# Kernel tuning notes

Hardware: AMD Instinct MI355X
Metric: run time of the kernel (lower is better)

## Reference

```python
import jax, jax.numpy as jnp
import numpy as np

N = 100000   # nodes
E = 1600000  # edges
H = 2        # heads
F = 64       # out_feats per head
D = 256      # node feature dim
DE = 8       # edge feature dim
NEG_SLOPE = 0.2


def setup_inputs() -> dict:
    key = jax.random.key(0)
    ks = jax.random.split(key, 12)
    s = 0.05
    return {
        "feat_src": jax.random.normal(ks[0], (N, D), jnp.float32),
        "feat_edge": jax.random.normal(ks[1], (E, DE), jnp.float32),
        "edge_src": jax.random.randint(ks[2], (E,), 0, N, jnp.int32),
        "edge_dst": jax.random.randint(ks[3], (E,), 0, N, jnp.int32),
        "W_src": jax.random.normal(ks[4], (H * F, D), jnp.float32) * s,
        "W_dst": jax.random.normal(ks[5], (H * F, D), jnp.float32) * s,
        "b_dst": jax.random.normal(ks[6], (H * F,), jnp.float32) * s,
        "W_attn_src": jax.random.normal(ks[7], (H, D), jnp.float32) * s,
        "W_attn_dst": jax.random.normal(ks[8], (H, D), jnp.float32) * s,
        "W_attn_edge": jax.random.normal(ks[9], (H, DE), jnp.float32) * s,
        "W_ngnn": jax.random.normal(ks[10], (H * F, H * F), jnp.float32) * s,
        "b_ngnn": jax.random.normal(ks[11], (H * F,), jnp.float32) * s,
    }


def reference(feat_src, feat_edge, edge_src, edge_dst,
              W_src, W_dst, b_dst, W_attn_src, W_attn_dst, W_attn_edge,
              W_ngnn, b_ngnn):
    # node projections (graph is not a block -> feat_dst = feat_src)
    h_src = (feat_src @ W_src.T).reshape(N, H, F)          # [N,H,F]
    h_dst = (feat_src @ W_dst.T + b_dst).reshape(N, H, F)  # residual branch

    # per-node attention logits [N,H]
    a_src = feat_src @ W_attn_src.T
    a_dst = feat_src @ W_attn_dst.T
    a_edge = feat_edge @ W_attn_edge.T                     # [E,H]

    # per-edge score: u_add_v + edge term, LeakyReLU
    e = a_src[edge_src] + a_dst[edge_dst] + a_edge         # [E,H]
    e = jnp.where(e >= 0, e, NEG_SLOPE * e)

    # edge softmax over incoming edges of each destination node
    m = jax.ops.segment_max(e, edge_dst, num_segments=N)   # [N,H]
    ex = jnp.exp(e - m[edge_dst])
    z = jax.ops.segment_sum(ex, edge_dst, num_segments=N)  # [N,H]
    a = ex / z[edge_dst]                                   # [E,H]

    # weighted gather-scatter aggregation: u_mul_e -> sum per dst
    msg = h_src[edge_src] * a[:, :, None]                  # [E,H,F]
    rst = jax.ops.segment_sum(msg, edge_dst, num_segments=N)  # [N,H,F]

    # ngnn layer + ReLU
    rst = rst.reshape(N, H * F)
    rst = jax.nn.relu(rst @ W_ngnn.T + b_ngnn)
    rst = rst.reshape(N, H, F)

    # residual connection via dst_fc
    rst = rst + h_dst
    return rst
```

## Files before the change

### kernel.cpp

```cpp
#include <hip/hip_runtime.h>
#include <hip/hip_bf16.h>
#include <math.h>

#define NN 100000
#define EE 1600000
#define DD 256
#define DEE 8
#define HF 128
#define NEG_SLOPE 0.2f
#define NBUCK 196
#define P1_EPB 1024

typedef __bf16 bf16x8 __attribute__((ext_vector_type(8)));
typedef float  f32x4  __attribute__((ext_vector_type(4)));

__device__ inline ushort f2bf(float f) {
    uint32_t x = __builtin_bit_cast(uint32_t, f);
    x += 0x7fffu + ((x >> 16) & 1u);
    return (ushort)(x >> 16);
}
__device__ inline float bf2f(ushort u) {
    uint32_t x = ((uint32_t)u) << 16;
    return __builtin_bit_cast(float, x);
}
__device__ inline float u2f(uint u) { return __builtin_bit_cast(float, u); }
__device__ inline uint f2u(float f) { return __builtin_bit_cast(uint, f); }
__device__ inline float lo_bf(uint p) { return __builtin_bit_cast(float, p << 16); }
__device__ inline float hi_bf(uint p) { return __builtin_bit_cast(float, p & 0xffff0000u); }

__device__ inline void load_lds16(const void* g, void* l) {
    __builtin_amdgcn_global_load_lds(
        (const __attribute__((address_space(1))) void*)g,
        (__attribute__((address_space(3))) void*)l, 16, 0, 0);
}

__global__ __launch_bounds__(256) void f2bf3_kernel(
    const float* __restrict__ wa, const float* __restrict__ wb,
    const float* __restrict__ wc,
    ushort* __restrict__ oa, ushort* __restrict__ ob, ushort* __restrict__ oc)
{
    int i = (blockIdx.x * 256 + threadIdx.x) * 4;
    const int na = HF * DD, nb2 = 2 * HF * DD, nc3 = 2 * HF * DD + HF * HF;
    const float* src; ushort* dst; int o;
    if (i < na)       { src = wa; dst = oa; o = i; }
    else if (i < nb2) { src = wb; dst = ob; o = i - na; }
    else if (i < nc3) { src = wc; dst = oc; o = i - nb2; }
    else return;
    float4 v = *(const float4*)(src + o);
    ushort4 u;
    u.x = f2bf(v.x); u.y = f2bf(v.y); u.z = f2bf(v.z); u.w = f2bf(v.w);
    *(ushort4*)(dst + o) = u;
}

template<int K>
__global__ __launch_bounds__(256) void mfma_gemm_dual(
    const ushort* __restrict__ W0,
    const ushort* __restrict__ W1,
    const ushort* __restrict__ Xb,
    const float*  __restrict__ bias1,
    ushort* __restrict__ out0, ushort* __restrict__ out1)
{
    __shared__ ushort As[2][128 * 32];
    __shared__ ushort Bs[64 * 32];

    const int tid  = threadIdx.x;
    const int lane = tid & 63, wv = tid >> 6;
    const int wm = wv >> 1, wn = wv & 1;
    const int r = lane & 15, quad = lane >> 4;
    const int m0 = blockIdx.x * 64;

    f32x4 acc[2][4][2] = {};

    for (int k0 = 0; k0 < K; k0 += 32) {
#pragma unroll
        for (int t = 0; t < 2; ++t) {
            int is  = wv + t * 4;
            int row = is * 16 + (lane >> 2);
            int ko  = k0 + (lane & 3) * 8;
            load_lds16(W0 + (size_t)row * K + ko, &As[0][is * 512]);
            load_lds16(W1 + (size_t)row * K + ko, &As[1][is * 512]);
        }
        {
            int is  = wv;
            int row = is * 16 + (lane >> 2);
            int ko  = k0 + (lane & 3) * 8;
            int gm = m0 + row; gm = gm < NN ? gm : NN - 1;
            load_lds16(Xb + (size_t)gm * K + ko, &Bs[is * 512]);
        }
        __syncthreads();
        bf16x8 a[2][4], b[2];
#pragma unroll
        for (int i = 0; i < 4; ++i) {
            a[0][i] = __builtin_bit_cast(bf16x8,
                      *(const f32x4*)&As[0][(wm * 64 + i * 16 + r) * 32 + quad * 8]);
            a[1][i] = __builtin_bit_cast(bf16x8,
                      *(const f32x4*)&As[1][(wm * 64 + i * 16 + r) * 32 + quad * 8]);
        }
#pragma unroll
        for (int j = 0; j < 2; ++j)
            b[j] = __builtin_bit_cast(bf16x8,
                   *(const f32x4*)&Bs[(wn * 32 + j * 16 + r) * 32 + quad * 8]);
#pragma unroll
        for (int s = 0; s < 2; ++s)
#pragma unroll
            for (int i = 0; i < 4; ++i)
#pragma unroll
                for (int j = 0; j < 2; ++j)
                    acc[s][i][j] = __builtin_amdgcn_mfma_f32_16x16x32_bf16(
                        a[s][i], b[j], acc[s][i][j], 0, 0, 0);
        __syncthreads();
    }

#pragma unroll
    for (int s = 0; s < 2; ++s) {
        ushort* outp = s ? out1 : out0;
#pragma unroll
        for (int i = 0; i < 4; ++i) {
            int fbase = wm * 64 + i * 16 + quad * 4;
            float4 bv = make_float4(0.f, 0.f, 0.f, 0.f);
            if (s == 1) bv = *(const float4*)(bias1 + fbase);
#pragma unroll
            for (int j = 0; j < 2; ++j) {
                int node = m0 + wn * 32 + j * 16 + r;
                if (node >= NN) continue;
                f32x4 v = acc[s][i][j];
                v[0] += bv.x; v[1] += bv.y; v[2] += bv.z; v[3] += bv.w;
                ushort4 o;
                o.x = f2bf(v[0]); o.y = f2bf(v[1]); o.z = f2bf(v[2]); o.w = f2bf(v[3]);
                *(ushort4*)(outp + (size_t)node * HF + fbase) = o;
            }
        }
    }
}

template<int K>
__global__ __launch_bounds__(256) void mfma_gemm_ngnn(
    const ushort* __restrict__ Wb,
    const ushort* __restrict__ Xb,
    const float*  __restrict__ bias,
    const ushort* __restrict__ resid,
    float* __restrict__ outp)
{
    __shared__ ushort As[128 * 32];
    __shared__ ushort Bs[128 * 32];

    const int tid  = threadIdx.x;
    const int lane = tid & 63, wv = tid >> 6;
    const int wm = wv >> 1, wn = wv & 1;
    const int r = lane & 15, quad = lane >> 4;
    const int m0 = blockIdx.x * 128;

    f32x4 acc[4][4] = {};

    for (int k0 = 0; k0 < K; k0 += 32) {
#pragma unroll
        for (int t = 0; t < 2; ++t) {
            int is  = wv + t * 4;
            int row = is * 16 + (lane >> 2);
            int ko  = k0 + (lane & 3) * 8;
            load_lds16(Wb + (size_t)row * K + ko, &As[is * 512]);
            int gm = m0 + row; gm = gm < NN ? gm : NN - 1;
            load_lds16(Xb + (size_t)gm * K + ko, &Bs[is * 512]);
        }
        __syncthreads();
        bf16x8 a[4], b[4];
#pragma unroll
        for (int i = 0; i < 4; ++i) {
            a[i] = __builtin_bit_cast(bf16x8,
                   *(const f32x4*)&As[(wm * 64 + i * 16 + r) * 32 + quad * 8]);
            b[i] = __builtin_bit_cast(bf16x8,
                   *(const f32x4*)&Bs[(wn * 64 + i * 16 + r) * 32 + quad * 8]);
        }
#pragma unroll
        for (int i = 0; i < 4; ++i)
#pragma unroll
            for (int j = 0; j < 4; ++j)
                acc[i][j] = __builtin_amdgcn_mfma_f32_16x16x32_bf16(
                    a[i], b[j], acc[i][j], 0, 0, 0);
        __syncthreads();
    }

#pragma unroll
    for (int i = 0; i < 4; ++i) {
        int fbase = wm * 64 + i * 16 + quad * 4;
        float4 bv = *(const float4*)(bias + fbase);
#pragma unroll
        for (int j = 0; j < 4; ++j) {
            int node = m0 + wn * 64 + j * 16 + r;
            if (node >= NN) continue;
            f32x4 v = acc[i][j];
            ushort4 rs = *(const ushort4*)(resid + (size_t)node * HF + fbase);
            float4 o;
            o.x = fmaxf(v[0] + bv.x, 0.f) + bf2f(rs.x);
            o.y = fmaxf(v[1] + bv.y, 0.f) + bf2f(rs.y);
            o.z = fmaxf(v[2] + bv.z, 0.f) + bf2f(rs.z);
            o.w = fmaxf(v[3] + bv.w, 0.f) + bf2f(rs.w);
            *(float4*)(outp + (size_t)node * HF + fbase) = o;
        }
    }
}

__global__ __launch_bounds__(256) void attn_logits_kernel(
    const float* __restrict__ feat,
    const float* __restrict__ Was, const float* __restrict__ Wad,
    float* __restrict__ a_src, float* __restrict__ a_dst,
    ushort* __restrict__ feat_bf)
{
    int wave = threadIdx.x >> 6, lane = threadIdx.x & 63;
    int node = blockIdx.x * 4 + wave;
    if (node >= NN) return;
    float4 f = *(const float4*)(feat + (size_t)node * DD + lane * 4);
    ushort4 fb;
    fb.x = f2bf(f.x); fb.y = f2bf(f.y); fb.z = f2bf(f.z); fb.w = f2bf(f.w);
    *(ushort4*)(feat_bf + (size_t)node * DD + lane * 4) = fb;

    float4 w0 = *(const float4*)(Was + 0 * DD + lane * 4);
    float4 w1 = *(const float4*)(Was + 1 * DD + lane * 4);
    float4 w2 = *(const float4*)(Wad + 0 * DD + lane * 4);
    float4 w3 = *(const float4*)(Wad + 1 * DD + lane * 4);
    float p0 = f.x * w0.x + f.y * w0.y + f.z * w0.z + f.w * w0.w;
    float p1 = f.x * w1.x + f.y * w1.y + f.z * w1.z + f.w * w1.w;
    float p2 = f.x * w2.x + f.y * w2.y + f.z * w2.z + f.w * w2.w;
    float p3 = f.x * w3.x + f.y * w3.y + f.z * w3.z + f.w * w3.w;
#pragma unroll
    for (int o = 32; o > 0; o >>= 1) {
        p0 += __shfl_xor(p0, o);
        p1 += __shfl_xor(p1, o);
        p2 += __shfl_xor(p2, o);
        p3 += __shfl_xor(p3, o);
    }
    if (lane == 0) {
        a_src[node * 2 + 0] = p0; a_src[node * 2 + 1] = p1;
        a_dst[node * 2 + 0] = p2; a_dst[node * 2 + 1] = p3;
    }
}

__global__ __launch_bounds__(256) void hist_kernel(
    const int* __restrict__ edge_dst, int* __restrict__ deg)
{
    int i = blockIdx.x * 256 + threadIdx.x;
    if (i < EE) atomicAdd(&deg[edge_dst[i]], 1);
}

#define SCAN_ELEMS 1024
__global__ __launch_bounds__(256) void scan1_kernel(
    const int* __restrict__ deg, int* __restrict__ offsets, int* __restrict__ blockSums)
{
    __shared__ int sd[256];
    int tid = threadIdx.x;
    int base = blockIdx.x * SCAN_ELEMS + tid * 4;
    int v[4];
#pragma unroll
    for (int c = 0; c < 4; ++c) v[c] = (base + c < NN) ? deg[base + c] : 0;
    int tsum = v[0] + v[1] + v[2] + v[3];
    sd[tid] = tsum;
    __syncthreads();
    for (int o = 1; o < 256; o <<= 1) {
        int x = (tid >= o) ? sd[tid - o] : 0;
        __syncthreads();
        sd[tid] += x;
        __syncthreads();
    }
    int excl = sd[tid] - tsum;
    int run = excl;
#pragma unroll
    for (int c = 0; c < 4; ++c) {
        if (base + c < NN) offsets[base + c] = run;
        run += v[c];
    }
    if (tid == 255) blockSums[blockIdx.x] = sd[255];
}

__global__ __launch_bounds__(128) void scan2_kernel(int* __restrict__ blockSums, int nb)
{
    __shared__ int sd[128];
    int tid = threadIdx.x;
    int tv = (tid < nb) ? blockSums[tid] : 0;
    sd[tid] = tv;
    __syncthreads();
    for (int o = 1; o < 128; o <<= 1) {
        int x = (tid >= o) ? sd[tid - o] : 0;
        __syncthreads();
        sd[tid] += x;
        __syncthreads();
    }
    if (tid < nb) blockSums[tid] = sd[tid] - tv;
}

__global__ __launch_bounds__(256) void scan3_kernel(
    int* __restrict__ offsets, const int* __restrict__ blockSums,
    int* __restrict__ bcur)
{
    int tid = threadIdx.x;
    int base = blockIdx.x * SCAN_ELEMS + tid * 4;
    int add = blockSums[blockIdx.x];
#pragma unroll
    for (int c = 0; c < 4; ++c) {
        int idx = base + c;
        if (idx < NN) {
            int v = offsets[idx] + add;
            offsets[idx] = v;
            if ((idx & 511) == 0) bcur[idx >> 9] = v;
        }
    }
    if (blockIdx.x == 0 && tid == 0) offsets[NN] = EE;
}

__global__ __launch_bounds__(256) void bucket_scatter_kernel(
    const int* __restrict__ edge_src, const int* __restrict__ edge_dst,
    const float* __restrict__ feat_edge,
    const float* __restrict__ a_src, const float* __restrict__ a_dst,
    const float* __restrict__ Wae,
    int* __restrict__ bcur, uint4* __restrict__ staging)
{
    __shared__ int cnt[256];
    __shared__ int basearr[256];
    __shared__ int run[256];
    const int tid = threadIdx.x;
    const int b0 = blockIdx.x * P1_EPB;

    cnt[tid] = 0;
    __syncthreads();
#pragma unroll
    for (int j = 0; j < P1_EPB / 256; ++j) {
        int i = b0 + j * 256 + tid;
        if (i < EE) atomicAdd(&cnt[edge_dst[i] >> 9], 1);
    }
    __syncthreads();
    if (tid < NBUCK) {
        int c = cnt[tid];
        basearr[tid] = c ? atomicAdd(&bcur[tid], c) : 0;
    }
    run[tid] = 0;
    __syncthreads();

    float4 w00 = ((const float4*)Wae)[0], w01 = ((const float4*)Wae)[1];
    float4 w10 = ((const float4*)Wae)[2], w11 = ((const float4*)Wae)[3];

#pragma unroll
    for (int j = 0; j < P1_EPB / 256; ++j) {
        int i = b0 + j * 256 + tid;
        if (i >= EE) continue;
        int s = edge_src[i], d = edge_dst[i];
        float4 e0 = ((const float4*)feat_edge)[i * 2 + 0];
        float4 e1 = ((const float4*)feat_edge)[i * 2 + 1];
        float ae0 = e0.x*w00.x + e0.y*w00.y + e0.z*w00.z + e0.w*w00.w
                  + e1.x*w01.x + e1.y*w01.y + e1.z*w01.z + e1.w*w01.w;
        float ae1 = e0.x*w10.x + e0.y*w10.y + e0.z*w10.z + e0.w*w10.w
                  + e1.x*w11.x + e1.y*w11.y + e1.z*w11.z + e1.w*w11.w;
        float v0 = a_src[s * 2 + 0] + a_dst[d * 2 + 0] + ae0;
        float v1 = a_src[s * 2 + 1] + a_dst[d * 2 + 1] + ae1;
        v0 = (v0 >= 0.f) ? v0 : NEG_SLOPE * v0;
        v1 = (v1 >= 0.f) ? v1 : NEG_SLOPE * v1;
        int bk = d >> 9;
        int ofs = atomicAdd(&run[bk], 1);
        staging[basearr[bk] + ofs] = make_uint4((uint)s, (uint)d, f2u(v0), f2u(v1));
    }
}

__global__ __launch_bounds__(256) void fine_scatter_kernel(
    const int* __restrict__ offsets,
    const uint4* __restrict__ staging, uint4* __restrict__ pairs)
{
    __shared__ int cur[512];
    const int tid = threadIdx.x;
    const int nb0 = blockIdx.x * 512;
    const int ncnt = (NN - nb0 < 512) ? (NN - nb0) : 512;
    for (int i = tid; i < ncnt; i += 256) cur[i] = offsets[nb0 + i];
    __syncthreads();
    const int lo = offsets[nb0];
    const int hi = offsets[nb0 + ncnt];
    for (int j = lo + tid; j < hi; j += 256) {
        uint4 it = staging[j];
        int n = (int)it.y - nb0;
        int pos = atomicAdd(&cur[n], 1);
        pairs[pos] = it;
    }
}

__global__ __launch_bounds__(256) void aggregate_fused(
    const int* __restrict__ offsets,
    const uint4* __restrict__ pairs,
    const ushort* __restrict__ hsrc,
    ushort* __restrict__ agg)
{
    __shared__ uint4 stash[4][64];
    int wave = threadIdx.x >> 6, lane = threadIdx.x & 63;
    int node = blockIdx.x * 4 + wave;
    if (node >= NN) return;
    int off = offsets[node], end = offsets[node + 1];
    int n = end - off;
    uint* aggw = (uint*)agg;
    if (n <= 0) { aggw[(size_t)node * 64 + lane] = 0; return; }
    const uint* h2 = (const uint*)hsrc;
    int hh = lane >> 5;

    float acc0 = 0.f, acc1 = 0.f, z0 = 0.f, z1 = 0.f;

    if (n <= 64) {
        uint4 pr = (lane < n) ? pairs[off + lane]
                              : make_uint4(0u, 0u, 0xff800000u, 0xff800000u);
        float m0 = u2f(pr.z), m1 = u2f(pr.w);
#pragma unroll
        for (int o = 32; o > 0; o >>= 1) {
            m0 = fmaxf(m0, __shfl_xor(m0, o));
            m1 = fmaxf(m1, __shfl_xor(m1, o));
        }
        float ex0 = (lane < n) ? __expf(u2f(pr.z) - m0) : 0.f;
        float ex1 = (lane < n) ? __expf(u2f(pr.w) - m1) : 0.f;
        z0 = ex0; z1 = ex1;
        stash[wave][lane] = make_uint4(pr.x, f2u(ex0), f2u(ex1), 0u);
        __builtin_amdgcn_wave_barrier();
#pragma unroll 4
        for (int k = 0; k < n; ++k) {
            uint4 st = stash[wave][k];
            uint p = h2[(size_t)st.x * 64 + lane];
            float w = hh ? u2f(st.z) : u2f(st.y);
            acc0 = fmaf(w, lo_bf(p), acc0);
            acc1 = fmaf(w, hi_bf(p), acc1);
        }
    } else {
        float m0 = -INFINITY, m1 = -INFINITY;
        for (int c0 = 0; c0 < n; c0 += 64) {
            if (c0 + lane < n) {
                uint4 pr = pairs[off + c0 + lane];
                m0 = fmaxf(m0, u2f(pr.z));
                m1 = fmaxf(m1, u2f(pr.w));
            }
        }
#pragma unroll
        for (int o = 32; o > 0; o >>= 1) {
            m0 = fmaxf(m0, __shfl_xor(m0, o));
            m1 = fmaxf(m1, __shfl_xor(m1, o));
        }
        for (int c0 = 0; c0 < n; c0 += 64) {
            int cn = n - c0; if (cn > 64) cn = 64;
            uint srcv = 0; float ex0 = 0.f, ex1 = 0.f;
            if (lane < cn) {
                uint4 pr = pairs[off + c0 + lane];
                srcv = pr.x;
                ex0 = __expf(u2f(pr.z) - m0);
                ex1 = __expf(u2f(pr.w) - m1);
                z0 += ex0; z1 += ex1;
            }
            stash[wave][lane] = make_uint4(srcv, f2u(ex0), f2u(ex1), 0u);
            __builtin_amdgcn_wave_barrier();
#pragma unroll 4
            for (int k = 0; k < cn; ++k) {
                uint4 st = stash[wave][k];
                uint p = h2[(size_t)st.x * 64 + lane];
                float w = hh ? u2f(st.z) : u2f(st.y);
                acc0 = fmaf(w, lo_bf(p), acc0);
                acc1 = fmaf(w, hi_bf(p), acc1);
            }
            __builtin_amdgcn_wave_barrier();
        }
    }

#pragma unroll
    for (int o = 32; o > 0; o >>= 1) {
        z0 += __shfl_xor(z0, o);
        z1 += __shfl_xor(z1, o);
    }
    float zi = hh ? ((z1 > 0.f) ? 1.f / z1 : 0.f)
                  : ((z0 > 0.f) ? 1.f / z0 : 0.f);
    float r0 = acc0 * zi;
    float r1 = acc1 * zi;
    aggw[(size_t)node * 64 + lane] = ((uint)f2bf(r1) << 16) | (uint)f2bf(r0);
}

extern "C" void kernel_launch(void* const* d_in, const int* in_sizes, int n_in,
                              void* d_out, int out_size, void* d_ws, size_t ws_size,
                              hipStream_t stream) {
    (void)in_sizes; (void)n_in; (void)out_size; (void)ws_size;
    const float* feat_src  = (const float*)d_in[0];
    const float* feat_edge = (const float*)d_in[1];
    const int*   edge_src  = (const int*)d_in[2];
    const int*   edge_dst  = (const int*)d_in[3];
    const float* W_src     = (const float*)d_in[4];
    const float* W_dst     = (const float*)d_in[5];
    const float* b_dst     = (const float*)d_in[6];
    const float* W_attn_src  = (const float*)d_in[7];
    const float* W_attn_dst  = (const float*)d_in[8];
    const float* W_attn_edge = (const float*)d_in[9];
    const float* W_ngnn    = (const float*)d_in[10];
    const float* b_ngnn    = (const float*)d_in[11];
    float* out = (float*)d_out;

    char* base = (char*)d_ws;
    size_t off = 0;
    auto take = [&](size_t bytes) -> void* {
        void* p = base + off;
        off = (off + bytes + 511) & ~(size_t)511;
        return p;
    };
    ushort* feat_bf  = (ushort*)take((size_t)NN * DD * 2);
    ushort* h_src_bf = (ushort*)take((size_t)NN * HF * 2);
    uint4*  staging  = (uint4*)take((size_t)EE * 16);
    uint4*  pairs    = (uint4*)take((size_t)EE * 16);
    float*  a_src_b  = (float*)take((size_t)NN * 2 * 4);
    float*  a_dst_b  = (float*)take((size_t)NN * 2 * 4);
    int*    deg      = (int*)take((size_t)NN * 4);
    int*    offsets  = (int*)take((size_t)(NN + 1) * 4);
    int*    bcur     = (int*)take((size_t)NBUCK * 4);
    int*    blockSums= (int*)take(512);
    ushort* Wsrc_bf  = (ushort*)take((size_t)HF * DD * 2);
    ushort* Wdst_bf  = (ushort*)take((size_t)HF * DD * 2);
    ushort* Wngnn_bf = (ushort*)take((size_t)HF * HF * 2);
    ushort* h_dst_bf = (ushort*)staging;
    ushort* agg_bf   = feat_bf;

    const int NB_SCAN = (NN + SCAN_ELEMS - 1) / SCAN_ELEMS;
    const int GB_E  = (EE + 255) / 256;
    const int GB_M  = (NN + 127) / 128;
    const int GB_M64= (NN + 63) / 64;
    const int GB_N4 = (NN + 3) / 4;
    const int GB_P1 = (EE + P1_EPB - 1) / P1_EPB;
    const int W3_N  = (2 * HF * DD + HF * HF) / 4;
    const int GB_W3 = (W3_N + 255) / 256;

    hipMemsetAsync(deg, 0, (size_t)NN * 4, stream);
    hipLaunchKernelGGL(hist_kernel, dim3(GB_E), dim3(256), 0, stream, edge_dst, deg);
    hipLaunchKernelGGL(scan1_kernel, dim3(NB_SCAN), dim3(256), 0, stream, deg, offsets, blockSums);
    hipLaunchKernelGGL(scan2_kernel, dim3(1), dim3(128), 0, stream, blockSums, NB_SCAN);
    hipLaunchKernelGGL(scan3_kernel, dim3(NB_SCAN), dim3(256), 0, stream, offsets, blockSums, bcur);

    hipLaunchKernelGGL(attn_logits_kernel, dim3(GB_N4), dim3(256), 0, stream,
                       feat_src, W_attn_src, W_attn_dst, a_src_b, a_dst_b, feat_bf);

    hipLaunchKernelGGL(f2bf3_kernel, dim3(GB_W3), dim3(256), 0, stream,
                       W_src, W_dst, W_ngnn, Wsrc_bf, Wdst_bf, Wngnn_bf);

    hipLaunchKernelGGL(bucket_scatter_kernel, dim3(GB_P1), dim3(256), 0, stream,
                       edge_src, edge_dst, feat_edge, a_src_b, a_dst_b, W_attn_edge,
                       bcur, staging);
    hipLaunchKernelGGL(fine_scatter_kernel, dim3(NBUCK), dim3(256), 0, stream,
                       offsets, staging, pairs);

    hipLaunchKernelGGL((mfma_gemm_dual<DD>), dim3(GB_M64), dim3(256), 0, stream,
                       Wsrc_bf, Wdst_bf, feat_bf, b_dst, h_src_bf, h_dst_bf);

    hipLaunchKernelGGL(aggregate_fused, dim3(GB_N4), dim3(256), 0, stream,
                       offsets, pairs, h_src_bf, agg_bf);

    hipLaunchKernelGGL((mfma_gemm_ngnn<HF>), dim3(GB_M), dim3(256), 0, stream,
                       Wngnn_bf, agg_bf, b_ngnn, h_dst_bf, out);
}
```

Measured before the change: 522.2 us.

## Stage bucket records in shared memory for coalesced staging writes

The coarse bucket scatter now sorts each block's edge records into LDS by bucket, using a block-wide prefix scan of the bucket counts, and then writes them to the global staging buffer in contiguous runs. Before, each record went straight to a scattered global address, so this targets the cost of uncoalesced stores. The change also doubles edges per block, keeps src/dst in registers instead of reloading them, and reads the attention logits as float2. In exchange it uses 32KB of LDS per block, which may lower occupancy, and adds a serial scan with many barriers.

```diff
diff --git a/kernel.cpp b/kernel.cpp
--- a/kernel.cpp
+++ b/kernel.cpp
@@ -9,7 +9,8 @@
 #define HF 128
 #define NEG_SLOPE 0.2f
 #define NBUCK 196
-#define P1_EPB 1024
+#define P1_EPB 2048
+#define P1_ITER (P1_EPB / 256)
 
 typedef __bf16 bf16x8 __attribute__((ext_vector_type(8)));
 typedef float  f32x4  __attribute__((ext_vector_type(4)));
@@ -313,48 +314,78 @@
     const float* __restrict__ Wae,
     int* __restrict__ bcur, uint4* __restrict__ staging)
 {
+    __shared__ uint4 rec[P1_EPB];
     __shared__ int cnt[256];
+    __shared__ int scanv[256];
+    __shared__ int cur[256];
     __shared__ int basearr[256];
-    __shared__ int run[256];
+
     const int tid = threadIdx.x;
     const int b0 = blockIdx.x * P1_EPB;
 
     cnt[tid] = 0;
     __syncthreads();
-#pragma unroll
-    for (int j = 0; j < P1_EPB / 256; ++j) {
+
+    int sA[P1_ITER], dA[P1_ITER];
+#pragma unroll
+    for (int j = 0; j < P1_ITER; ++j) {
         int i = b0 + j * 256 + tid;
-        if (i < EE) atomicAdd(&cnt[edge_dst[i] >> 9], 1);
-    }
-    __syncthreads();
-    if (tid < NBUCK) {
-        int c = cnt[tid];
-        basearr[tid] = c ? atomicAdd(&bcur[tid], c) : 0;
-    }
-    run[tid] = 0;
+        int s = 0, d = 0;
+        if (i < EE) {
+            s = edge_src[i];
+            d = edge_dst[i];
+            atomicAdd(&cnt[d >> 9], 1);
+        }
+        sA[j] = s; dA[j] = d;
+    }
+    __syncthreads();
+
+    int c = cnt[tid];
+    scanv[tid] = c;
+    __syncthreads();
+    for (int o = 1; o < 256; o <<= 1) {
+        int x = (tid >= o) ? scanv[tid - o] : 0;
+        __syncthreads();
+        scanv[tid] += x;
+        __syncthreads();
+    }
+    int excl = scanv[tid] - c;
+    cur[tid] = excl;
+    if (tid < NBUCK) basearr[tid] = c ? atomicAdd(&bcur[tid], c) : 0;
+    scanv[tid] = excl;
     __syncthreads();
 
     float4 w00 = ((const float4*)Wae)[0], w01 = ((const float4*)Wae)[1];
     float4 w10 = ((const float4*)Wae)[2], w11 = ((const float4*)Wae)[3];
 
 #pragma unroll
-    for (int j = 0; j < P1_EPB / 256; ++j) {
+    for (int j = 0; j < P1_ITER; ++j) {
         int i = b0 + j * 256 + tid;
         if (i >= EE) continue;
-        int s = edge_src[i], d = edge_dst[i];
+        int s = sA[j], d = dA[j];
         float4 e0 = ((const float4*)feat_edge)[i * 2 + 0];
         float4 e1 = ((const float4*)feat_edge)[i * 2 + 1];
         float ae0 = e0.x*w00.x + e0.y*w00.y + e0.z*w00.z + e0.w*w00.w
                   + e1.x*w01.x + e1.y*w01.y + e1.z*w01.z + e1.w*w01.w;
         float ae1 = e0.x*w10.x + e0.y*w10.y + e0.z*w10.z + e0.w*w10.w
                   + e1.x*w11.x + e1.y*w11.y + e1.z*w11.z + e1.w*w11.w;
-        float v0 = a_src[s * 2 + 0] + a_dst[d * 2 + 0] + ae0;
-        float v1 = a_src[s * 2 + 1] + a_dst[d * 2 + 1] + ae1;
+        float2 as = ((const float2*)a_src)[s];
+        float2 ad = ((const float2*)a_dst)[d];
+        float v0 = as.x + ad.x + ae0;
+        float v1 = as.y + ad.y + ae1;
         v0 = (v0 >= 0.f) ? v0 : NEG_SLOPE * v0;
         v1 = (v1 >= 0.f) ? v1 : NEG_SLOPE * v1;
         int bk = d >> 9;
-        int ofs = atomicAdd(&run[bk], 1);
-        staging[basearr[bk] + ofs] = make_uint4((uint)s, (uint)d, f2u(v0), f2u(v1));
+        int pos = atomicAdd(&cur[bk], 1);
+        rec[pos] = make_uint4((uint)s, (uint)d, f2u(v0), f2u(v1));
+    }
+    __syncthreads();
+
+    const int tot = (EE - b0 < P1_EPB) ? (EE - b0) : P1_EPB;
+    for (int idx = tid; idx < tot; idx += 256) {
+        uint4 r = rec[idx];
+        int bk = (int)(r.y >> 9);
+        staging[basearr[bk] + (idx - scanv[bk])] = r;
     }
 }
 
@@ -543,6 +574,6 @@
     hipLaunchKernelGGL(aggregate_fused, dim3(GB_N4), dim3(256), 0, stream,
                        offsets, pairs, h_src_bf, agg_bf);
 
-    hipLaunchKernelGGL((mfma_gemm_ngnn<HF>), dim3(GB_M), dim3(256), 0, stream,
+    hipLaunchKernelGGL(mfma_gemm_ngnn<HF>, dim3(GB_M), dim3(256), 0, stream,
                        Wngnn_bf, agg_bf, b_ngnn, h_dst_bf, out);
 }
```

After: 496.7 us. 4.9% less time.
